# Kernel optimization log

Measured on AMD Instinct MI355X. Metric: run time of the kernel, lower is better.

The kernel has to match this reference:

```python
import jax, jax.numpy as jnp
import numpy as np

IN_F = 4096
OUT_F = 4096
RANK = 8
NUM_EXPERTS = 64
TOP_K = 16
ROUTER_DIM = 16
ALPHA = 32
SCALING = ALPHA / TOP_K
BOTTLENECK = NUM_EXPERTS * RANK


def setup_inputs() -> dict:
    key = jax.random.key(0)
    ks = jax.random.split(key, 5)
    x = jax.random.normal(ks[0], (4, 4096, IN_F), dtype=jnp.float32)
    # kaiming-uniform-ish A, random B (zeros init would make output trivially 0)
    bound_a = float(np.sqrt(6.0 / IN_F))
    A_w = jax.random.uniform(ks[1], (BOTTLENECK, IN_F), jnp.float32, -bound_a, bound_a)
    B_w = jax.random.normal(ks[2], (OUT_F, BOTTLENECK), dtype=jnp.float32) * 0.02
    Wq_w = jax.random.normal(ks[3], (ROUTER_DIM, IN_F), dtype=jnp.float32) * 0.02
    keys = jax.random.normal(ks[4], (NUM_EXPERTS, ROUTER_DIM), dtype=jnp.float32) * 0.01
    return {"x": x, "A_w": A_w, "B_w": B_w, "Wq_w": Wq_w, "keys": keys}


def reference(x, A_w, B_w, Wq_w, keys):
    # lowrank router: q = x @ Wq^T, scores = q @ keys^T  -> [B,S,E]
    q = jnp.einsum('bsd,rd->bsr', x, Wq_w)
    scores = jnp.einsum('bsr,er->bse', q, keys)
    top_vals, top_idx = jax.lax.top_k(scores, TOP_K)          # [B,S,K]
    top_w = jax.nn.softmax(top_vals, axis=-1)                 # [B,S,K]
    # scatter weights into dense gate over experts [B,S,E]
    gate = jnp.sum(jax.nn.one_hot(top_idx, NUM_EXPERTS, dtype=top_w.dtype)
                   * top_w[..., None], axis=-2)
    # shared low-rank down-proj, gated per expert, up-proj
    z = jnp.einsum('bsd,nd->bsn', x, A_w)                     # [B,S,E*r]
    z = z.reshape(*z.shape[:-1], NUM_EXPERTS, RANK)
    z_gated = (z * gate[..., None]).reshape(*z.shape[:-2], BOTTLENECK)
    out = jnp.einsum('bsn,on->bso', z_gated, B_w) * SCALING
    return out
```

## Files before the change

### kernel.cpp

```cpp
#include <hip/hip_runtime.h>
#include <hip/hip_bf16.h>
#include <stdint.h>

#define IN_F 4096
#define OUT_F 4096
#define NE 64
#define TOPK 16
#define RD 16
#define BOT 512
#define NTOK 16384

typedef __attribute__((ext_vector_type(8))) short short8;
typedef __attribute__((ext_vector_type(4))) float floatx4;

__device__ __forceinline__ unsigned short f2bf_ru(float f) {
  unsigned int u = __float_as_uint(f);
  return (unsigned short)((u + 0x8000u) >> 16);
}
__device__ __forceinline__ unsigned short f2bf_rne(float f) {
  unsigned int u = __float_as_uint(f);
  return (unsigned short)((u + 0x7FFFu + ((u >> 16) & 1u)) >> 16);
}

__device__ __forceinline__ void gl2lds16(const void* g, void* l) {
  __builtin_amdgcn_global_load_lds(
      (const __attribute__((address_space(1))) unsigned int*)g,
      (__attribute__((address_space(3))) unsigned int*)l, 16, 0, 0);
}

__global__ __launch_bounds__(256) void prep_kernel(
    const float* __restrict__ A_w, const float* __restrict__ B_w,
    unsigned short* __restrict__ Abf, unsigned short* __restrict__ Bbf) {
  int i = blockIdx.x * 256 + threadIdx.x;
  if (i < BOT * IN_F) {
    Abf[i] = f2bf_rne(A_w[i]);
    Bbf[i] = f2bf_rne(B_w[i]);
  }
}

__global__ __launch_bounds__(256) void router_kernel(
    const float* __restrict__ x, const float* __restrict__ Wq,
    const float* __restrict__ keys, float* __restrict__ gate,
    unsigned short* __restrict__ xbf, int write_xbf) {
  __shared__ double qp[32][16][8];
  __shared__ double q_lds[32][16];
  __shared__ double sc[32][64];
  const int tid = threadIdx.x;
  const size_t t0 = (size_t)blockIdx.x * 32;
  const int tg = tid >> 3;
  const int r8 = tid & 7;
  const size_t row = t0 + tg;

  double acc[16];
#pragma unroll
  for (int r = 0; r < 16; r++) acc[r] = 0.0;

  const float* xr = x + row * IN_F;
  unsigned short* xbr = xbf + row * IN_F;

  for (int c = 0; c < 128; c++) {
    const int k = (c * 8 + r8) * 4;
    float4 v = *(const float4*)(xr + k);
    if (write_xbf) {
      ushort4 h;
      h.x = f2bf_ru(v.x); h.y = f2bf_ru(v.y);
      h.z = f2bf_ru(v.z); h.w = f2bf_ru(v.w);
      *(ushort4*)(xbr + k) = h;
    }
#pragma unroll
    for (int r = 0; r < 16; r++) {
      float4 wv = *(const float4*)(Wq + (size_t)r * IN_F + k);
      acc[r] += (double)v.x * (double)wv.x;
      acc[r] += (double)v.y * (double)wv.y;
      acc[r] += (double)v.z * (double)wv.z;
      acc[r] += (double)v.w * (double)wv.w;
    }
  }
#pragma unroll
  for (int r = 0; r < 16; r++) qp[tg][r][r8] = acc[r];
  __syncthreads();

  {
    int token = tid >> 3, rr = tid & 7;
    for (int h = 0; h < 2; h++) {
      int r = rr + h * 8;
      double s = 0.0;
      for (int p = 0; p < 8; p++) s += qp[token][r][p];
      q_lds[token][r] = s;
    }
  }
  __syncthreads();

  {
    int t = tid >> 3, e0 = (tid & 7) * 8;
    for (int e = e0; e < e0 + 8; e++) {
      double s = 0.0;
      for (int rr = 0; rr < 16; rr++) s += q_lds[t][rr] * (double)keys[e * RD + rr];
      sc[t][e] = s;
    }
  }
  __syncthreads();

  if (tid < 32) {
    int t = tid;
    double vals[16]; int idx[16];
    unsigned long long used = 0ull;
    for (int s = 0; s < 16; s++) {
      double best = -1e300; int bi = 0;
      for (int e = 0; e < 64; e++) {
        double v = sc[t][e];
        if (!((used >> e) & 1ull) && v > best) { best = v; bi = e; }
      }
      used |= (1ull << bi);
      vals[s] = best; idx[s] = bi;
    }
    double mx = vals[0], sum = 0.0, wv[16];
    for (int i = 0; i < 16; i++) { wv[i] = exp(vals[i] - mx); sum += wv[i]; }
    double inv = 1.0 / sum;
    float* grow = gate + (t0 + t) * NE;
    for (int e = 0; e < 64; e++) grow[e] = 0.0f;
    for (int i = 0; i < 16; i++) grow[idx[i]] = (float)(wv[i] * inv);
  }
}

__global__ __launch_bounds__(256) void stageA_fast(
    const unsigned short* __restrict__ xbf, const unsigned short* __restrict__ Abf,
    const float* __restrict__ gate, unsigned short* __restrict__ z) {
  __shared__ unsigned short As[128 * 32];
  __shared__ unsigned short Bs[128 * 32];
  __shared__ float gl[128 * 16];
  const int tid = threadIdx.x;
  const int bid = blockIdx.x;
  const int xc = bid & 7, ii = bid >> 3;
  const int mt = xc * 16 + (ii >> 2);
  const int nt = ii & 3;
  const size_t m0 = (size_t)mt * 128;
  const int n0 = nt * 128;
  const int wid = tid >> 6, lane = tid & 63;

  for (int i = 0; i < 8; i++) {
    int f = i * 256 + tid;
    gl[f] = gate[(m0 + (f >> 4)) * NE + (n0 >> 3) + (f & 15)];
  }
  const int wm = (wid & 1) * 64, wn = (wid >> 1) * 64;
  const int lr = lane & 15, lq = lane >> 4;
  floatx4 acc[4][4];
  for (int i = 0; i < 4; i++)
    for (int j = 0; j < 4; j++) acc[i][j] = 0.0f;

  const int q0 = wid * 64 + lane;
  const int r0 = q0 >> 2, c0 = (q0 & 3) * 8;
  const int q1 = 256 + q0;
  const int r1 = q1 >> 2, c1 = (q1 & 3) * 8;
  const unsigned short* gA0 = xbf + (m0 + r0) * IN_F + c0;
  const unsigned short* gA1 = xbf + (m0 + r1) * IN_F + c1;
  const unsigned short* gB0 = Abf + (size_t)(n0 + r0) * IN_F + c0;
  const unsigned short* gB1 = Abf + (size_t)(n0 + r1) * IN_F + c1;
  unsigned short* lA0 = As + (wid * 64) * 8;
  unsigned short* lA1 = As + (256 + wid * 64) * 8;
  unsigned short* lB0 = Bs + (wid * 64) * 8;
  unsigned short* lB1 = Bs + (256 + wid * 64) * 8;

  for (int k0 = 0; k0 < IN_F; k0 += 32) {
    gl2lds16(gA0 + k0, lA0);
    gl2lds16(gA1 + k0, lA1);
    gl2lds16(gB0 + k0, lB0);
    gl2lds16(gB1 + k0, lB1);
    __syncthreads();
    short8 a[4], b[4];
    for (int i = 0; i < 4; i++) a[i] = *(const short8*)(As + (wm + i * 16 + lr) * 32 + lq * 8);
    for (int j = 0; j < 4; j++) b[j] = *(const short8*)(Bs + (wn + j * 16 + lr) * 32 + lq * 8);
    for (int i = 0; i < 4; i++)
      for (int j = 0; j < 4; j++)
        acc[i][j] = __builtin_amdgcn_mfma_f32_16x16x32_bf16(a[i], b[j], acc[i][j], 0, 0, 0);
    __syncthreads();
  }
  for (int i = 0; i < 4; i++) {
    for (int j = 0; j < 4; j++) {
      int cl = wn + j * 16 + lr;
      int el = cl >> 3;
      for (int g = 0; g < 4; g++) {
        int rl = wm + i * 16 + lq * 4 + g;
        float v = acc[i][j][g] * gl[rl * 16 + el];
        z[(m0 + rl) * BOT + n0 + cl] = f2bf_ru(v);
      }
    }
  }
}

__global__ __launch_bounds__(256) void stageA_kernel(
    const float* __restrict__ x, const unsigned short* __restrict__ Abf,
    const float* __restrict__ gate, unsigned short* __restrict__ z) {
  __shared__ unsigned short As[128 * 32];
  __shared__ unsigned short Bs[128 * 32];
  __shared__ float gl[128 * 16];
  const int tid = threadIdx.x;
  const int bid = blockIdx.x;
  const int mt = (bid & 7) + (bid >> 5) * 8;
  const int nt = (bid >> 3) & 3;
  const size_t m0 = (size_t)mt * 128;
  const int n0 = nt * 128;

  for (int i = 0; i < 8; i++) {
    int f = i * 256 + tid;
    gl[f] = gate[(m0 + (f >> 4)) * NE + (n0 >> 3) + (f & 15)];
  }
  const int wid = tid >> 6, lane = tid & 63;
  const int wm = (wid & 1) * 64, wn = (wid >> 1) * 64;
  const int lr = lane & 15, lq = lane >> 4;
  floatx4 acc[4][4];
  for (int i = 0; i < 4; i++)
    for (int j = 0; j < 4; j++) acc[i][j] = 0.0f;

  for (int k0 = 0; k0 < IN_F; k0 += 32) {
    __syncthreads();
    {
      int c4 = (tid & 7) * 4;
      int rbase = tid >> 3;
      for (int p = 0; p < 4; p++) {
        int row = p * 32 + rbase;
        float4 v = *(const float4*)(x + (m0 + row) * IN_F + k0 + c4);
        ushort4 h;
        h.x = f2bf_ru(v.x); h.y = f2bf_ru(v.y);
        h.z = f2bf_ru(v.z); h.w = f2bf_ru(v.w);
        *(ushort4*)(As + row * 32 + c4) = h;
      }
    }
    for (int p = 0; p < 2; p++) {
      int f = p * 256 + tid;
      int row = f >> 2, c8 = (f & 3) * 8;
      float4 v = *(const float4*)(Abf + (size_t)(n0 + row) * IN_F + k0 + c8);
      *(float4*)(Bs + row * 32 + c8) = v;
    }
    __syncthreads();
    short8 a[4], b[4];
    for (int i = 0; i < 4; i++) a[i] = *(const short8*)(As + (wm + i * 16 + lr) * 32 + lq * 8);
    for (int j = 0; j < 4; j++) b[j] = *(const short8*)(Bs + (wn + j * 16 + lr) * 32 + lq * 8);
    for (int i = 0; i < 4; i++)
      for (int j = 0; j < 4; j++)
        acc[i][j] = __builtin_amdgcn_mfma_f32_16x16x32_bf16(a[i], b[j], acc[i][j], 0, 0, 0);
  }
  for (int i = 0; i < 4; i++) {
    for (int j = 0; j < 4; j++) {
      int cl = wn + j * 16 + lr;
      int el = cl >> 3;
      for (int g = 0; g < 4; g++) {
        int rl = wm + i * 16 + lq * 4 + g;
        float v = acc[i][j][g] * gl[rl * 16 + el];
        z[(m0 + rl) * BOT + n0 + cl] = f2bf_ru(v);
      }
    }
  }
}

__global__ __launch_bounds__(256) void stageB_fast(
    const unsigned short* __restrict__ z, const unsigned short* __restrict__ Bbf,
    float* __restrict__ out) {
  __shared__ unsigned short As[128 * 32];
  __shared__ unsigned short Bs[128 * 32];
  const int tid = threadIdx.x;
  const int bid = blockIdx.x;
  const int xc = bid & 7, ii = bid >> 3;
  const int mt = xc * 16 + (ii >> 5);
  const int nt = ii & 31;
  const size_t m0 = (size_t)mt * 128;
  const int n0 = nt * 128;
  const int wid = tid >> 6, lane = tid & 63;
  const int wm = (wid & 1) * 64, wn = (wid >> 1) * 64;
  const int lr = lane & 15, lq = lane >> 4;
  floatx4 acc[4][4];
  for (int i = 0; i < 4; i++)
    for (int j = 0; j < 4; j++) acc[i][j] = 0.0f;

  const int q0 = wid * 64 + lane;
  const int r0 = q0 >> 2, c0 = (q0 & 3) * 8;
  const int q1 = 256 + q0;
  const int r1 = q1 >> 2, c1 = (q1 & 3) * 8;
  const unsigned short* gA0 = z + (m0 + r0) * BOT + c0;
  const unsigned short* gA1 = z + (m0 + r1) * BOT + c1;
  const unsigned short* gB0 = Bbf + (size_t)(n0 + r0) * BOT + c0;
  const unsigned short* gB1 = Bbf + (size_t)(n0 + r1) * BOT + c1;
  unsigned short* lA0 = As + (wid * 64) * 8;
  unsigned short* lA1 = As + (256 + wid * 64) * 8;
  unsigned short* lB0 = Bs + (wid * 64) * 8;
  unsigned short* lB1 = Bs + (256 + wid * 64) * 8;

  for (int k0 = 0; k0 < BOT; k0 += 32) {
    gl2lds16(gA0 + k0, lA0);
    gl2lds16(gA1 + k0, lA1);
    gl2lds16(gB0 + k0, lB0);
    gl2lds16(gB1 + k0, lB1);
    __syncthreads();
    short8 a[4], b[4];
    for (int i = 0; i < 4; i++) a[i] = *(const short8*)(As + (wm + i * 16 + lr) * 32 + lq * 8);
    for (int j = 0; j < 4; j++) b[j] = *(const short8*)(Bs + (wn + j * 16 + lr) * 32 + lq * 8);
    for (int i = 0; i < 4; i++)
      for (int j = 0; j < 4; j++)
        acc[i][j] = __builtin_amdgcn_mfma_f32_16x16x32_bf16(a[i], b[j], acc[i][j], 0, 0, 0);
    __syncthreads();
  }
  for (int i = 0; i < 4; i++) {
    for (int j = 0; j < 4; j++) {
      int cl = wn + j * 16 + lr;
      for (int g = 0; g < 4; g++) {
        int rl = wm + i * 16 + lq * 4 + g;
        out[(m0 + rl) * OUT_F + n0 + cl] = acc[i][j][g] * 2.0f;
      }
    }
  }
}

extern "C" void kernel_launch(void* const* d_in, const int* in_sizes, int n_in,
                              void* d_out, int out_size, void* d_ws, size_t ws_size,
                              hipStream_t stream) {
  const float* x    = (const float*)d_in[0];
  const float* A_w  = (const float*)d_in[1];
  const float* B_w  = (const float*)d_in[2];
  const float* Wq   = (const float*)d_in[3];
  const float* keys = (const float*)d_in[4];
  float* out = (float*)d_out;

  char* ws = (char*)d_ws;
  float* gate          = (float*)ws;
  unsigned short* zbuf = (unsigned short*)(ws + (4 << 20));
  unsigned short* Abf  = (unsigned short*)(ws + (20 << 20));
  unsigned short* Bbf  = (unsigned short*)(ws + (24 << 20));
  unsigned short* xbf  = (unsigned short*)(ws + (28 << 20));
  const int fast = ws_size >= ((size_t)156 << 20);

  hipLaunchKernelGGL(prep_kernel, dim3(8192), dim3(256), 0, stream, A_w, B_w, Abf, Bbf);
  hipLaunchKernelGGL(router_kernel, dim3(512), dim3(256), 0, stream, x, Wq, keys, gate,
                     xbf, fast);
  if (fast)
    hipLaunchKernelGGL(stageA_fast, dim3(512), dim3(256), 0, stream, xbf, Abf, gate, zbuf);
  else
    hipLaunchKernelGGL(stageA_kernel, dim3(512), dim3(256), 0, stream, x, Abf, gate, zbuf);
  hipLaunchKernelGGL(stageB_fast, dim3(4096), dim3(256), 0, stream, zbuf, Bbf, out);
}
```

Measured before the change: 852.7 us.

## Stage Wq chunks in LDS and reuse across two tokens per thread in router

Measured after the change: 934.8 us. 9.6% more time.

```diff
diff --git a/kernel.cpp b/kernel.cpp
--- a/kernel.cpp
+++ b/kernel.cpp
@@ -42,51 +42,75 @@
     const float* __restrict__ x, const float* __restrict__ Wq,
     const float* __restrict__ keys, float* __restrict__ gate,
     unsigned short* __restrict__ xbf, int write_xbf) {
-  __shared__ double qp[32][16][8];
+  __shared__ float wq_lds[16][512];
   __shared__ double q_lds[32][16];
   __shared__ double sc[32][64];
   const int tid = threadIdx.x;
   const size_t t0 = (size_t)blockIdx.x * 32;
-  const int tg = tid >> 3;
-  const int r8 = tid & 7;
-  const size_t row = t0 + tg;
-
-  double acc[16];
-#pragma unroll
-  for (int r = 0; r < 16; r++) acc[r] = 0.0;
-
-  const float* xr = x + row * IN_F;
-  unsigned short* xbr = xbf + row * IN_F;
-
-  for (int c = 0; c < 128; c++) {
-    const int k = (c * 8 + r8) * 4;
-    float4 v = *(const float4*)(xr + k);
-    if (write_xbf) {
-      ushort4 h;
-      h.x = f2bf_ru(v.x); h.y = f2bf_ru(v.y);
-      h.z = f2bf_ru(v.z); h.w = f2bf_ru(v.w);
-      *(ushort4*)(xbr + k) = h;
-    }
+  const int s = tid & 15;
+  const int tg = tid >> 4;
+  const size_t row0 = t0 + 2 * tg;
+  const size_t row1 = row0 + 1;
+  const float* xr0 = x + row0 * IN_F;
+  const float* xr1 = x + row1 * IN_F;
+  unsigned short* xb0 = xbf + row0 * IN_F;
+  unsigned short* xb1 = xbf + row1 * IN_F;
+
+  double acc0[16], acc1[16];
+#pragma unroll
+  for (int r = 0; r < 16; r++) { acc0[r] = 0.0; acc1[r] = 0.0; }
+
+  for (int kc = 0; kc < IN_F; kc += 512) {
+    __syncthreads();
+#pragma unroll
+    for (int i = 0; i < 8; i++) {
+      int f = i * 256 + tid;
+      int rr = f >> 7, cc = (f & 127) * 4;
+      *(float4*)(&wq_lds[rr][cc]) = *(const float4*)(Wq + (size_t)rr * IN_F + kc + cc);
+    }
+    __syncthreads();
+#pragma unroll
+    for (int i = 0; i < 8; i++) {
+      const int kk = (i * 16 + s) * 4;
+      float4 v0 = *(const float4*)(xr0 + kc + kk);
+      float4 v1 = *(const float4*)(xr1 + kc + kk);
+      if (write_xbf) {
+        ushort4 h0, h1;
+        h0.x = f2bf_ru(v0.x); h0.y = f2bf_ru(v0.y);
+        h0.z = f2bf_ru(v0.z); h0.w = f2bf_ru(v0.w);
+        h1.x = f2bf_ru(v1.x); h1.y = f2bf_ru(v1.y);
+        h1.z = f2bf_ru(v1.z); h1.w = f2bf_ru(v1.w);
+        *(ushort4*)(xb0 + kc + kk) = h0;
+        *(ushort4*)(xb1 + kc + kk) = h1;
+      }
+#pragma unroll
+      for (int r = 0; r < 16; r++) {
+        float4 wv = *(const float4*)(&wq_lds[r][kk]);
+        acc0[r] += (double)v0.x * (double)wv.x;
+        acc0[r] += (double)v0.y * (double)wv.y;
+        acc0[r] += (double)v0.z * (double)wv.z;
+        acc0[r] += (double)v0.w * (double)wv.w;
+        acc1[r] += (double)v1.x * (double)wv.x;
+        acc1[r] += (double)v1.y * (double)wv.y;
+        acc1[r] += (double)v1.z * (double)wv.z;
+        acc1[r] += (double)v1.w * (double)wv.w;
+      }
+    }
+  }
+
+#pragma unroll
+  for (int m = 1; m < 16; m <<= 1) {
 #pragma unroll
     for (int r = 0; r < 16; r++) {
-      float4 wv = *(const float4*)(Wq + (size_t)r * IN_F + k);
-      acc[r] += (double)v.x * (double)wv.x;
-      acc[r] += (double)v.y * (double)wv.y;
-      acc[r] += (double)v.z * (double)wv.z;
-      acc[r] += (double)v.w * (double)wv.w;
-    }
-  }
-#pragma unroll
-  for (int r = 0; r < 16; r++) qp[tg][r][r8] = acc[r];
-  __syncthreads();
-
-  {
-    int token = tid >> 3, rr = tid & 7;
-    for (int h = 0; h < 2; h++) {
-      int r = rr + h * 8;
-      double s = 0.0;
-      for (int p = 0; p < 8; p++) s += qp[token][r][p];
-      q_lds[token][r] = s;
+      acc0[r] += __shfl_xor(acc0[r], m, 64);
+      acc1[r] += __shfl_xor(acc1[r], m, 64);
+    }
+  }
+  if (s == 0) {
+#pragma unroll
+    for (int r = 0; r < 16; r++) {
+      q_lds[2 * tg][r] = acc0[r];
+      q_lds[2 * tg + 1][r] = acc1[r];
     }
   }
   __syncthreads();
@@ -94,9 +118,9 @@
   {
     int t = tid >> 3, e0 = (tid & 7) * 8;
     for (int e = e0; e < e0 + 8; e++) {
-      double s = 0.0;
-      for (int rr = 0; rr < 16; rr++) s += q_lds[t][rr] * (double)keys[e * RD + rr];
-      sc[t][e] = s;
+      double sv = 0.0;
+      for (int rr = 0; rr < 16; rr++) sv += q_lds[t][rr] * (double)keys[e * RD + rr];
+      sc[t][e] = sv;
     }
   }
   __syncthreads();
@@ -105,14 +129,14 @@
     int t = tid;
     double vals[16]; int idx[16];
     unsigned long long used = 0ull;
-    for (int s = 0; s < 16; s++) {
+    for (int st = 0; st < 16; st++) {
       double best = -1e300; int bi = 0;
       for (int e = 0; e < 64; e++) {
         double v = sc[t][e];
         if (!((used >> e) & 1ull) && v > best) { best = v; bi = e; }
       }
       used |= (1ull << bi);
-      vals[s] = best; idx[s] = bi;
+      vals[st] = best; idx[st] = bi;
     }
     double mx = vals[0], sum = 0.0, wv[16];
     for (int i = 0; i < 16; i++) { wv[i] = exp(vals[i] - mx); sum += wv[i]; }
```

## Transpose Wq to fp64 in prep and restructure router dot-product partitioning

Applied to the files above, without the earlier changes.

After: 1.132 ms. 1.33x slower.

```diff
diff --git a/kernel.cpp b/kernel.cpp
--- a/kernel.cpp
+++ b/kernel.cpp
@@ -30,73 +30,65 @@
 
 __global__ __launch_bounds__(256) void prep_kernel(
     const float* __restrict__ A_w, const float* __restrict__ B_w,
-    unsigned short* __restrict__ Abf, unsigned short* __restrict__ Bbf) {
+    const float* __restrict__ Wq,
+    unsigned short* __restrict__ Abf, unsigned short* __restrict__ Bbf,
+    double* __restrict__ wq64T) {
   int i = blockIdx.x * 256 + threadIdx.x;
   if (i < BOT * IN_F) {
     Abf[i] = f2bf_rne(A_w[i]);
     Bbf[i] = f2bf_rne(B_w[i]);
   }
+  if (i < RD * IN_F) {
+    int r = i & 15, k = i >> 4;
+    wq64T[i] = (double)Wq[(size_t)r * IN_F + k];
+  }
 }
 
 __global__ __launch_bounds__(256) void router_kernel(
-    const float* __restrict__ x, const float* __restrict__ Wq,
+    const float* __restrict__ x, const double* __restrict__ wq64T,
     const float* __restrict__ keys, float* __restrict__ gate,
     unsigned short* __restrict__ xbf, int write_xbf) {
-  __shared__ double qp[32][16][8];
   __shared__ double q_lds[32][16];
   __shared__ double sc[32][64];
   const int tid = threadIdx.x;
   const size_t t0 = (size_t)blockIdx.x * 32;
-  const int tg = tid >> 3;
-  const int r8 = tid & 7;
-  const size_t row = t0 + tg;
-
-  double acc[16];
-#pragma unroll
-  for (int r = 0; r < 16; r++) acc[r] = 0.0;
-
+  const int w = tid >> 6, lane = tid & 63;
+  const int tIn = w * 8 + (lane >> 3);
+  const int r0 = (lane & 7) * 2;
+  const size_t row = t0 + tIn;
   const float* xr = x + row * IN_F;
-  unsigned short* xbr = xbf + row * IN_F;
-
-  for (int c = 0; c < 128; c++) {
-    const int k = (c * 8 + r8) * 4;
+  unsigned short* xb = xbf + row * IN_F;
+  const double* wt = wq64T + r0;
+
+  double a0 = 0.0, a1 = 0.0;
+#pragma unroll 2
+  for (int k = 0; k < IN_F; k += 4) {
     float4 v = *(const float4*)(xr + k);
     if (write_xbf) {
       ushort4 h;
       h.x = f2bf_ru(v.x); h.y = f2bf_ru(v.y);
       h.z = f2bf_ru(v.z); h.w = f2bf_ru(v.w);
-      *(ushort4*)(xbr + k) = h;
-    }
-#pragma unroll
-    for (int r = 0; r < 16; r++) {
-      float4 wv = *(const float4*)(Wq + (size_t)r * IN_F + k);
-      acc[r] += (double)v.x * (double)wv.x;
-      acc[r] += (double)v.y * (double)wv.y;
-      acc[r] += (double)v.z * (double)wv.z;
-      acc[r] += (double)v.w * (double)wv.w;
-    }
-  }
-#pragma unroll
-  for (int r = 0; r < 16; r++) qp[tg][r][r8] = acc[r];
-  __syncthreads();
-
-  {
-    int token = tid >> 3, rr = tid & 7;
-    for (int h = 0; h < 2; h++) {
-      int r = rr + h * 8;
-      double s = 0.0;
-      for (int p = 0; p < 8; p++) s += qp[token][r][p];
-      q_lds[token][r] = s;
-    }
-  }
+      *(ushort4*)(xb + k) = h;
+    }
+    double2 w0 = *(const double2*)(wt + (size_t)(k + 0) * 16);
+    double2 w1 = *(const double2*)(wt + (size_t)(k + 1) * 16);
+    double2 w2 = *(const double2*)(wt + (size_t)(k + 2) * 16);
+    double2 w3 = *(const double2*)(wt + (size_t)(k + 3) * 16);
+    a0 += (double)v.x * w0.x; a1 += (double)v.x * w0.y;
+    a0 += (double)v.y * w1.x; a1 += (double)v.y * w1.y;
+    a0 += (double)v.z * w2.x; a1 += (double)v.z * w2.y;
+    a0 += (double)v.w * w3.x; a1 += (double)v.w * w3.y;
+  }
+  q_lds[tIn][r0] = a0;
+  q_lds[tIn][r0 + 1] = a1;
   __syncthreads();
 
   {
     int t = tid >> 3, e0 = (tid & 7) * 8;
     for (int e = e0; e < e0 + 8; e++) {
-      double s = 0.0;
-      for (int rr = 0; rr < 16; rr++) s += q_lds[t][rr] * (double)keys[e * RD + rr];
-      sc[t][e] = s;
+      double sv = 0.0;
+      for (int rr = 0; rr < 16; rr++) sv += q_lds[t][rr] * (double)keys[e * RD + rr];
+      sc[t][e] = sv;
     }
   }
   __syncthreads();
@@ -105,14 +97,14 @@
     int t = tid;
     double vals[16]; int idx[16];
     unsigned long long used = 0ull;
-    for (int s = 0; s < 16; s++) {
+    for (int st = 0; st < 16; st++) {
       double best = -1e300; int bi = 0;
       for (int e = 0; e < 64; e++) {
         double v = sc[t][e];
         if (!((used >> e) & 1ull) && v > best) { best = v; bi = e; }
       }
       used |= (1ull << bi);
-      vals[s] = best; idx[s] = bi;
+      vals[st] = best; idx[st] = bi;
     }
     double mx = vals[0], sum = 0.0, wv[16];
     for (int i = 0; i < 16; i++) { wv[i] = exp(vals[i] - mx); sum += wv[i]; }
@@ -323,13 +315,14 @@
   char* ws = (char*)d_ws;
   float* gate          = (float*)ws;
   unsigned short* zbuf = (unsigned short*)(ws + (4 << 20));
+  double* wq64T        = (double*)(ws + (4 << 20));
   unsigned short* Abf  = (unsigned short*)(ws + (20 << 20));
   unsigned short* Bbf  = (unsigned short*)(ws + (24 << 20));
   unsigned short* xbf  = (unsigned short*)(ws + (28 << 20));
   const int fast = ws_size >= ((size_t)156 << 20);
 
-  hipLaunchKernelGGL(prep_kernel, dim3(8192), dim3(256), 0, stream, A_w, B_w, Abf, Bbf);
-  hipLaunchKernelGGL(router_kernel, dim3(512), dim3(256), 0, stream, x, Wq, keys, gate,
+  hipLaunchKernelGGL(prep_kernel, dim3(8192), dim3(256), 0, stream, A_w, B_w, Wq, Abf, Bbf, wq64T);
+  hipLaunchKernelGGL(router_kernel, dim3(512), dim3(256), 0, stream, x, wq64T, keys, gate,
                      xbf, fast);
   if (fast)
     hipLaunchKernelGGL(stageA_fast, dim3(512), dim3(256), 0, stream, xbf, Abf, gate, zbuf);
```
